# Performance work log

Measured on AMD Instinct MI355X. Metric: run time of the kernel, lower is better.

The kernel has to match this reference:

```python
import jax, jax.numpy as jnp
import numpy as np
import math

D = 2048          # embedding_size
H = 16            # nheads
HD = D // H       # head_dim
S = 2048          # seq_len
B = 2
# SwiGLU hidden per source: int(2*(4*D)/3) rounded up to multiple of 256
FF = 256 * ((int(2 * (4 * D) / 3) + 255) // 256)  # 5632
EPS = 1e-6


def pe_row(seq_len, d_model):
    # PositionalEncoding buffer, but forward uses only pe[:, seq_len-1]
    pos = float(seq_len - 1)
    div = jnp.exp(jnp.arange(0, d_model, 2, dtype=jnp.float32) * (-math.log(10000.0) / d_model))
    row = jnp.zeros((d_model,), jnp.float32)
    row = row.at[0::2].set(jnp.sin(pos * div))
    row = row.at[1::2].set(jnp.cos(pos * div))
    return row  # [D]


def rmsnorm(x, g, eps=EPS):
    xf = x.astype(jnp.float32)
    n = xf * jax.lax.rsqrt(jnp.mean(xf * xf, axis=-1, keepdims=True) + eps)
    return g * n.astype(x.dtype)


def setup_inputs() -> dict:
    key = jax.random.key(0)
    ks = jax.random.split(key, 16)
    sd = 0.02
    x = jax.random.normal(ks[0], (B, S, D), jnp.float32)
    mask = jnp.triu(jnp.ones((S, S), jnp.int32), k=1)[None, None]  # [1,1,S,S], 1 = masked
    return {
        'x': x,
        'mask': mask,
        'qkv_w': jax.random.normal(ks[1], (3 * D, D), jnp.float32) * sd,
        'qkv_b': jnp.zeros((3 * D,), jnp.float32),
        'fc_w': jax.random.normal(ks[2], (D, D), jnp.float32) * sd,
        'fc_b': jnp.zeros((D,), jnp.float32),
        'w1': jax.random.normal(ks[3], (FF, D), jnp.float32) * sd,
        'b1': jnp.zeros((FF,), jnp.float32),
        'w2': jax.random.normal(ks[4], (FF, D), jnp.float32) * sd,
        'b2': jnp.zeros((FF,), jnp.float32),
        'w3': jax.random.normal(ks[5], (D, FF), jnp.float32) * sd,
        'b3': jnp.zeros((D,), jnp.float32),
        'g_attn': jnp.ones((D,), jnp.float32),
        'g_ff': jnp.ones((D,), jnp.float32),
    }


def _block(x, mask, qkv_w, qkv_b, fc_w, fc_b, w1, b1, w2, b2, w3, b3, g_attn, g_ff):
    b, s, _ = x.shape
    # attention sublayer (pre-norm)
    h_in = rmsnorm(x, g_attn)
    qkv = h_in @ qkv_w.T + qkv_b
    xq, xk, xv = jnp.split(qkv, 3, axis=-1)
    pe = pe_row(s, D)  # single row added everywhere (faithful to source)
    xq = xq + pe
    xk = xk + pe
    q = xq.reshape(b, s, H, HD).transpose(0, 2, 1, 3)
    k = xk.reshape(b, s, H, HD).transpose(0, 2, 1, 3)
    v = xv.reshape(b, s, H, HD).transpose(0, 2, 1, 3)
    scores = jnp.einsum('bhqd,bhkd->bhqk', q, k) / math.sqrt(HD)
    scores = jnp.where(mask == 1, jnp.float32(-1e9), scores)
    attn = jax.nn.softmax(scores, axis=-1)
    out = jnp.einsum('bhqk,bhkd->bhqd', attn, v)
    out = out.transpose(0, 2, 1, 3).reshape(b, s, D)
    attn_out = out @ fc_w.T + fc_b
    h = x + attn_out
    # SwiGLU FFN sublayer (pre-norm)
    f_in = rmsnorm(h, g_ff)
    gate = jax.nn.silu(f_in @ w1.T + b1) * (f_in @ w2.T + b2)
    return h + gate @ w3.T + b3


def reference(x, mask, qkv_w, qkv_b, fc_w, fc_b, w1, b1, w2, b2, w3, b3, g_attn, g_ff):
    return _block(x, mask, qkv_w, qkv_b, fc_w, fc_b, w1, b1, w2, b2, w3, b3, g_attn, g_ff)
```

## Files before the change

kernel.cpp:

```cpp
#include <hip/hip_runtime.h>
#include <math.h>


typedef __attribute__((ext_vector_type(8))) short bf16x8;
typedef __attribute__((ext_vector_type(4))) short bf16x4;
typedef __attribute__((ext_vector_type(4))) float f32x4;

#define DEVI __device__ __forceinline__

DEVI unsigned short f2bf(float f) {
  unsigned u = __builtin_bit_cast(unsigned, f);
  u += 0x7FFFu + ((u >> 16) & 1u);
  return (unsigned short)(u >> 16);
}
DEVI float bf2f(unsigned short h) {
  unsigned u = ((unsigned)h) << 16;
  return __builtin_bit_cast(float, u);
}

#define GLL16(g, l) __builtin_amdgcn_global_load_lds( \
    (const __attribute__((address_space(1))) unsigned int*)(const void*)(g), \
    (__attribute__((address_space(3))) unsigned int*)(void*)(l), 16, 0, 0)

__global__ __launch_bounds__(256) void wconv_k(const float* __restrict__ src,
                                               unsigned short* __restrict__ dst,
                                               long n8) {
  long t = (long)blockIdx.x * 256 + threadIdx.x;
  if (t >= n8) return;
  const f32x4* s = (const f32x4*)(src + t * 8);
  f32x4 a = s[0], b = s[1];
  bf16x8 o;
#pragma unroll
  for (int j = 0; j < 4; ++j) {
    o[j]     = (short)f2bf(a[j]);
    o[4 + j] = (short)f2bf(b[j]);
  }
  *(bf16x8*)(dst + t * 8) = o;
}

__global__ void pe_k(float* __restrict__ pe) {
  int c = blockIdx.x * 256 + threadIdx.x;
  if (c >= 2048) return;
  int i2 = c & ~1;
  float div = __expf(-(float)i2 * (9.210340371976184f / 2048.0f));
  float ang = 2047.0f * div;
  pe[c] = (c & 1) ? cosf(ang) : sinf(ang);
}

__global__ __launch_bounds__(256) void rmsnorm_k(const float* __restrict__ x,
                                                 const float* __restrict__ g,
                                                 unsigned short* __restrict__ out) {
  long row = blockIdx.x;
  const float* xr = x + row * 2048;
  int tid = threadIdx.x;
  f32x4 v0 = *(const f32x4*)&xr[tid * 8];
  f32x4 v1 = *(const f32x4*)&xr[tid * 8 + 4];
  float ss = 0.f;
#pragma unroll
  for (int j = 0; j < 4; ++j) ss += v0[j] * v0[j] + v1[j] * v1[j];
#pragma unroll
  for (int m = 1; m < 64; m <<= 1) ss += __shfl_xor(ss, m, 64);
  __shared__ float red[4];
  int lane = tid & 63, wv = tid >> 6;
  if (lane == 0) red[wv] = ss;
  __syncthreads();
  float tot = red[0] + red[1] + red[2] + red[3];
  float rn = rsqrtf(tot * (1.0f / 2048.0f) + 1e-6f);
  const float* gr = g + tid * 8;
  bf16x8 o;
#pragma unroll
  for (int j = 0; j < 4; ++j) {
    o[j]     = (short)f2bf(v0[j] * rn * gr[j]);
    o[4 + j] = (short)f2bf(v1[j] * rn * gr[4 + j]);
  }
  *(bf16x8*)&out[row * 2048 + tid * 8] = o;
}

template <int EPI>
__global__ __launch_bounds__(256) void gemm_bt(const unsigned short* __restrict__ A,
                                               const unsigned short* __restrict__ W,
                                               const float* __restrict__ bias,
                                               const void* __restrict__ residv,
                                               void* __restrict__ outv,
                                               int M, int N, int K) {
  __shared__ __align__(16) unsigned short Ab[3][4096];
  __shared__ __align__(16) unsigned short Bb[3][4096];
  const int tid  = threadIdx.x;
  const int lane = tid & 63;
  const int wv   = tid >> 6;
  const int wr   = wv >> 1;
  const int wc   = wv & 1;
  const int l15  = lane & 15;
  const int lg   = lane >> 4;
  const long tm  = (long)blockIdx.y * 128;
  const long tn  = (long)blockIdx.x * 128;

  const int srw = tid >> 2;
  const int sch = ((tid & 3) ^ ((srw >> 1) & 3)) << 3;
  const unsigned short* gA = A + (tm + srw) * (long)K + sch;
  const unsigned short* gB = W + (tn + srw) * (long)K + sch;
  const long rowstep = 64L * K;

#define STG(slot, kt) do {                                          \
    GLL16(gA + ((long)(kt) << 5), &Ab[slot][wv * 512]);             \
    GLL16(gA + rowstep + ((long)(kt) << 5), &Ab[slot][2048 + wv * 512]); \
    GLL16(gB + ((long)(kt) << 5), &Bb[slot][wv * 512]);             \
    GLL16(gB + rowstep + ((long)(kt) << 5), &Bb[slot][2048 + wv * 512]); \
  } while (0)

  const int KT = K >> 5;
  STG(0, 0); STG(1, 1);
  asm volatile("s_waitcnt vmcnt(4)" ::: "memory");
  __builtin_amdgcn_s_barrier();

  f32x4 acc[4][4] = {};
  const int sw = ((lg ^ ((l15 >> 1) & 3)) << 3);

  for (int t = 0; t < KT; ++t) {
    const unsigned short* lA = &Ab[t % 3][0];
    const unsigned short* lB = &Bb[t % 3][0];
    bf16x8 af[4], bfv[4];
#pragma unroll
    for (int m = 0; m < 4; ++m)
      af[m] = *(const bf16x8*)&lA[(wr * 64 + m * 16 + l15) * 32 + sw];
#pragma unroll
    for (int n = 0; n < 4; ++n)
      bfv[n] = *(const bf16x8*)&lB[(wc * 64 + n * 16 + l15) * 32 + sw];
    if (t + 2 < KT) STG((t + 2) % 3, t + 2);
    __builtin_amdgcn_s_setprio(1);
#pragma unroll
    for (int m = 0; m < 4; ++m)
#pragma unroll
      for (int n = 0; n < 4; ++n)
        acc[m][n] = __builtin_amdgcn_mfma_f32_16x16x32_bf16(af[m], bfv[n], acc[m][n], 0, 0, 0);
    __builtin_amdgcn_s_setprio(0);
    if (t + 2 < KT)      asm volatile("s_waitcnt vmcnt(4)" ::: "memory");
    else if (t + 1 < KT) asm volatile("s_waitcnt vmcnt(0)" ::: "memory");
    __builtin_amdgcn_s_barrier();
  }
#undef STG
  __builtin_amdgcn_sched_barrier(0);

  const long row0 = tm + wr * 64 + ((lane >> 4) << 2);
  const long col0 = tn + wc * 64;
#pragma unroll
  for (int n = 0; n < 4; ++n) {
    const long col = col0 + n * 16 + l15;
    const float bv = bias[col];
#pragma unroll
    for (int m = 0; m < 4; ++m) {
      const long rw = row0 + m * 16;
#pragma unroll
      for (int j = 0; j < 4; ++j) {
        const float v = acc[m][n][j] + bv;
        const long i = (rw + j) * (long)N + col;
        if (EPI == 0) {
          ((unsigned short*)outv)[i] = f2bf(v);
        } else if (EPI == 1) {
          ((float*)outv)[i] = ((const float*)residv)[i] + v;
        } else {
          float f1 = bf2f(((const unsigned short*)residv)[i]);
          float sg = f1 / (1.0f + __expf(-f1));
          ((unsigned short*)outv)[i] = f2bf(sg * v);
        }
      }
    }
  }
}

__global__ __launch_bounds__(256) void krepack_k(const unsigned short* __restrict__ qkv,
                                                 const float* __restrict__ pe,
                                                 unsigned short* __restrict__ kpe) {
  long t = (long)blockIdx.x * 256 + threadIdx.x;
  long idx = t * 8;
  long row = idx >> 11;
  int cd  = (int)(idx & 2047);
  int h = cd >> 7, d = cd & 127;
  long b = row >> 11, s = row & 2047;
  bf16x8 v = *(const bf16x8*)&qkv[row * 6144 + 2048 + cd];
  const float* per = &pe[cd];
#pragma unroll
  for (int j = 0; j < 8; ++j)
    v[j] = (short)f2bf(bf2f((unsigned short)v[j]) + per[j]);
  *(bf16x8*)&kpe[(((b * 16 + h)) * 2048 + s) * 128 + d] = v;
}

__global__ __launch_bounds__(256) void vtrans_k(const unsigned short* __restrict__ qkv,
                                                unsigned short* __restrict__ Vt) {
  const int s0 = blockIdx.x * 64;
  const int d0 = blockIdx.y * 64;
  const int bh = blockIdx.z;
  const long b = bh >> 4;
  const int h = bh & 15;
  __shared__ unsigned short tile[64][76];
  const int t = threadIdx.x;
#pragma unroll
  for (int half = 0; half < 2; ++half) {
    int c = t + half * 256;
    int r = c >> 3;
    int cc = (c & 7) * 8;
    bf16x8 v = *(const bf16x8*)&qkv[(b * 2048 + s0 + r) * 6144 + 4096 + h * 128 + d0 + cc];
#pragma unroll
    for (int j = 0; j < 8; ++j) tile[cc + j][r] = (unsigned short)v[j];
  }
  __syncthreads();
#pragma unroll
  for (int half = 0; half < 2; ++half) {
    int c = t + half * 256;
    int dr = c >> 3;
    int sc = (c & 7) * 8;
    bf16x4 lo = *(const bf16x4*)&tile[dr][sc];
    bf16x4 hi = *(const bf16x4*)&tile[dr][sc + 4];
    bf16x8 v;
#pragma unroll
    for (int j = 0; j < 4; ++j) { v[j] = lo[j]; v[4 + j] = hi[j]; }
    *(bf16x8*)&Vt[((long)bh * 128 + d0 + dr) * 2048 + s0 + sc] = v;
  }
}

__global__ __launch_bounds__(256, 2) void fattn_k(const unsigned short* __restrict__ QKV,
                                                  const float* __restrict__ pe,
                                                  const unsigned short* __restrict__ Kp,
                                                  const unsigned short* __restrict__ Vt,
                                                  unsigned short* __restrict__ O) {
  const int lin = blockIdx.x;
  const int chunk = lin & 7;
  const int idx = lin >> 3;
  const int bh = chunk * 4 + (idx >> 4);
  const int i16 = idx & 15;
  const int qb = (i16 & 1) ? ((i16 - 1) >> 1) : (15 - (i16 >> 1));
  const long b = bh >> 4;
  const int h = bh & 15;
  const int q0 = qb * 128;
  const int tid = threadIdx.x, lane = tid & 63, wv = tid >> 6;
  const int l15 = lane & 15, lg = lane >> 4;
  const int qw = q0 + wv * 32;

  __shared__ __align__(16) unsigned short Kl[2][8192];
  __shared__ __align__(16) unsigned short Vl[2][8192];
  __shared__ __align__(16) unsigned short Plds[4][32][40];

  const float scale = 0.08838834764831845f;
  const unsigned short* Qb = QKV + (b * 2048 + qw) * 6144 + h * 128;
  bf16x8 qf[2][4];
#pragma unroll
  for (int r = 0; r < 2; ++r)
#pragma unroll
    for (int kc = 0; kc < 4; ++kc) {
      bf16x8 v = *(const bf16x8*)&Qb[(r * 16 + l15) * 6144 + kc * 32 + lg * 8];
      const float* per = &pe[h * 128 + kc * 32 + lg * 8];
#pragma unroll
      for (int j = 0; j < 8; ++j)
        v[j] = (short)f2bf((bf2f((unsigned short)v[j]) + per[j]) * scale);
      qf[r][kc] = v;
    }

  const unsigned short* Kg = Kp + (long)bh * 2048 * 128;
  const unsigned short* Vg = Vt + (long)bh * 128 * 2048;

  auto stage = [&](int buf, int key0) {
#pragma unroll
    for (int ld = 0; ld < 4; ++ld) {
      int sr = wv * 16 + ld * 4 + (lane >> 4);
      int sc = ((lane & 15) << 3) ^ ((sr & 7) << 3);
      GLL16(Kg + (long)(key0 + sr) * 128 + sc, &Kl[buf][wv * 2048 + ld * 512]);
      int dr = wv * 32 + ld * 8 + (lane >> 3);
      int dc = ((lane & 7) << 3) ^ ((dr & 7) << 3);
      GLL16(Vg + (long)dr * 2048 + key0 + dc, &Vl[buf][wv * 2048 + ld * 512]);
    }
  };

  f32x4 o[2][8] = {};
  float mr[2][4], sdn[2][4];
#pragma unroll
  for (int r = 0; r < 2; ++r)
#pragma unroll
    for (int j = 0; j < 4; ++j) { mr[r][j] = -1e30f; sdn[r][j] = 0.f; }

  const int nkt = (q0 >> 6) + 2;
  stage(0, 0);
  __syncthreads();
  int cur = 0;
  for (int kt = 0; kt < nkt; ++kt) {
    const int key0 = kt << 6;
    if (kt + 1 < nkt) stage(cur ^ 1, key0 + 64);
    if (key0 <= qw + 31) {
      f32x4 s[2][4] = {};
      __builtin_amdgcn_s_setprio(1);
#pragma unroll
      for (int ks = 0; ks < 4; ++ks) {
        bf16x8 kf[4];
#pragma unroll
        for (int kc = 0; kc < 4; ++kc)
          kf[kc] = *(const bf16x8*)&Kl[cur][(ks * 16 + l15) * 128 +
                                           ((kc * 32 + lg * 8) ^ ((l15 & 7) << 3))];
#pragma unroll
        for (int r = 0; r < 2; ++r)
#pragma unroll
          for (int kc = 0; kc < 4; ++kc)
            s[r][ks] = __builtin_amdgcn_mfma_f32_16x16x32_bf16(qf[r][kc], kf[kc], s[r][ks], 0, 0, 0);
      }
      __builtin_amdgcn_s_setprio(0);
      const bool maskt = (key0 + 63 > qw);
      float pm[2][4];
#pragma unroll
      for (int r = 0; r < 2; ++r)
#pragma unroll
        for (int j = 0; j < 4; ++j) pm[r][j] = -1e30f;
#pragma unroll
      for (int r = 0; r < 2; ++r)
#pragma unroll
        for (int ks = 0; ks < 4; ++ks)
#pragma unroll
          for (int j = 0; j < 4; ++j) {
            float v = s[r][ks][j];
            if (maskt) {
              int qrow = qw + r * 16 + lg * 4 + j;
              int key  = key0 + ks * 16 + l15;
              v = (key <= qrow) ? v : -1e30f;
              s[r][ks][j] = v;
            }
            pm[r][j] = fmaxf(pm[r][j], v);
          }
#pragma unroll
      for (int msk = 1; msk < 16; msk <<= 1)
#pragma unroll
        for (int r = 0; r < 2; ++r)
#pragma unroll
          for (int j = 0; j < 4; ++j) pm[r][j] = fmaxf(pm[r][j], __shfl_xor(pm[r][j], msk, 64));
      bool grow = false;
#pragma unroll
      for (int r = 0; r < 2; ++r)
#pragma unroll
        for (int j = 0; j < 4; ++j) grow = grow || (pm[r][j] > mr[r][j] + 8.0f);
      if (__any(grow)) {
#pragma unroll
        for (int r = 0; r < 2; ++r)
#pragma unroll
          for (int j = 0; j < 4; ++j) {
            float mn = fmaxf(mr[r][j], pm[r][j]);
            float corr = __expf(mr[r][j] - mn);
            mr[r][j] = mn;
            sdn[r][j] *= corr;
#pragma unroll
            for (int nf = 0; nf < 8; ++nf) o[r][nf][j] *= corr;
          }
      }
      float ps[2][4];
#pragma unroll
      for (int r = 0; r < 2; ++r)
#pragma unroll
        for (int j = 0; j < 4; ++j) ps[r][j] = 0.f;
#pragma unroll
      for (int r = 0; r < 2; ++r)
#pragma unroll
        for (int ks = 0; ks < 4; ++ks)
#pragma unroll
          for (int j = 0; j < 4; ++j) {
            float e = __expf(s[r][ks][j] - mr[r][j]);
            s[r][ks][j] = e;
            ps[r][j] += e;
          }
#pragma unroll
      for (int msk = 1; msk < 16; msk <<= 1)
#pragma unroll
        for (int r = 0; r < 2; ++r)
#pragma unroll
          for (int j = 0; j < 4; ++j) ps[r][j] += __shfl_xor(ps[r][j], msk, 64);
#pragma unroll
      for (int r = 0; r < 2; ++r)
#pragma unroll
        for (int j = 0; j < 4; ++j) sdn[r][j] += ps[r][j];
#pragma unroll
      for (int hk = 0; hk < 2; ++hk) {
#pragma unroll
        for (int r = 0; r < 2; ++r)
#pragma unroll
          for (int ks2 = 0; ks2 < 2; ++ks2)
#pragma unroll
            for (int j = 0; j < 4; ++j)
              Plds[wv][r * 16 + lg * 4 + j][ks2 * 16 + l15] = f2bf(s[r][hk * 2 + ks2][j]);
        bf16x8 pf[2];
#pragma unroll
        for (int r = 0; r < 2; ++r) {
          bf16x4 lo = *(const bf16x4*)&Plds[wv][r * 16 + l15][lg * 8];
          bf16x4 hi = *(const bf16x4*)&Plds[wv][r * 16 + l15][lg * 8 + 4];
          bf16x8 p;
#pragma unroll
          for (int j = 0; j < 4; ++j) { p[j] = lo[j]; p[4 + j] = hi[j]; }
          pf[r] = p;
        }
        __builtin_amdgcn_s_setprio(1);
#pragma unroll
        for (int nf = 0; nf < 8; ++nf) {
          bf16x8 vf = *(const bf16x8*)&Vl[cur][(nf * 16 + l15) * 64 +
                                              ((hk * 32 + lg * 8) ^ ((l15 & 7) << 3))];
#pragma unroll
          for (int r = 0; r < 2; ++r)
            o[r][nf] = __builtin_amdgcn_mfma_f32_16x16x32_bf16(pf[r], vf, o[r][nf], 0, 0, 0);
        }
        __builtin_amdgcn_s_setprio(0);
      }
    }
    __syncthreads();
    cur ^= 1;
  }
  unsigned short* Ob = O + (b * 2048 + qw) * 2048 + h * 128;
#pragma unroll
  for (int r = 0; r < 2; ++r)
#pragma unroll
    for (int j = 0; j < 4; ++j) {
      float inv = 1.0f / sdn[r][j];
#pragma unroll
      for (int nf = 0; nf < 8; ++nf)
        Ob[(long)(r * 16 + lg * 4 + j) * 2048 + nf * 16 + l15] = f2bf(o[r][nf][j] * inv);
    }
}

extern "C" void kernel_launch(void* const* d_in, const int* in_sizes, int n_in,
                              void* d_out, int out_size, void* d_ws, size_t ws_size,
                              hipStream_t stream) {
  (void)in_sizes; (void)n_in; (void)out_size; (void)ws_size;
  const float* x    = (const float*)d_in[0];
  const float* qkvw = (const float*)d_in[2];
  const float* qkvb = (const float*)d_in[3];
  const float* fcw  = (const float*)d_in[4];
  const float* fcb  = (const float*)d_in[5];
  const float* w1   = (const float*)d_in[6];
  const float* b1   = (const float*)d_in[7];
  const float* w2   = (const float*)d_in[8];
  const float* b2   = (const float*)d_in[9];
  const float* w3   = (const float*)d_in[10];
  const float* b3   = (const float*)d_in[11];
  const float* ga   = (const float*)d_in[12];
  const float* gf   = (const float*)d_in[13];

  char* ws = (char*)d_ws;
  size_t off = 0;
  auto alloc = [&](size_t bytes) -> char* {
    char* p = ws + off;
    off = (off + bytes + 255) & ~(size_t)255;
    return p;
  };
  unsigned short* wqkv  = (unsigned short*)alloc(6144L * 2048 * 2);
  unsigned short* wfc   = (unsigned short*)alloc(2048L * 2048 * 2);
  unsigned short* w1b   = (unsigned short*)alloc(5632L * 2048 * 2);
  unsigned short* w2b   = (unsigned short*)alloc(5632L * 2048 * 2);
  unsigned short* w3b   = (unsigned short*)alloc(2048L * 5632 * 2);
  float*          pe    = (float*)alloc(2048 * 4);
  unsigned short* hin   = (unsigned short*)alloc(4096L * 2048 * 2);
  unsigned short* qkv   = (unsigned short*)alloc(4096L * 6144 * 2);
  unsigned short* kpe   = (unsigned short*)alloc(4096L * 2048 * 2);
  unsigned short* Vt    = (unsigned short*)alloc(4096L * 2048 * 2);
  unsigned short* attnb = (unsigned short*)alloc(4096L * 2048 * 2);
  float* h = (float*)d_out;

  wconv_k<<<6144, 256, 0, stream>>>(qkvw, wqkv, 6144L * 2048 / 8);
  wconv_k<<<2048, 256, 0, stream>>>(fcw,  wfc,  2048L * 2048 / 8);
  wconv_k<<<5632, 256, 0, stream>>>(w1,   w1b,  5632L * 2048 / 8);
  wconv_k<<<5632, 256, 0, stream>>>(w2,   w2b,  5632L * 2048 / 8);
  wconv_k<<<5632, 256, 0, stream>>>(w3,   w3b,  2048L * 5632 / 8);
  pe_k<<<8, 256, 0, stream>>>(pe);

  rmsnorm_k<<<4096, 256, 0, stream>>>(x, ga, hin);
  gemm_bt<0><<<dim3(48, 32), 256, 0, stream>>>(hin, wqkv, qkvb, nullptr, qkv, 4096, 6144, 2048);
  krepack_k<<<4096, 256, 0, stream>>>(qkv, pe, kpe);
  vtrans_k<<<dim3(32, 2, 32), 256, 0, stream>>>(qkv, Vt);
  fattn_k<<<dim3(512), 256, 0, stream>>>(qkv, pe, kpe, Vt, attnb);
  gemm_bt<1><<<dim3(16, 32), 256, 0, stream>>>(attnb, wfc, fcb, x, h, 4096, 2048, 2048);

  rmsnorm_k<<<4096, 256, 0, stream>>>(h, gf, hin);
  unsigned short* a1 = qkv;
  gemm_bt<0><<<dim3(44, 32), 256, 0, stream>>>(hin, w1b, b1, nullptr, a1, 4096, 5632, 2048);
  gemm_bt<2><<<dim3(44, 32), 256, 0, stream>>>(hin, w2b, b2, a1, a1, 4096, 5632, 2048);
  gemm_bt<1><<<dim3(16, 32), 256, 0, stream>>>(a1, w3b, b3, h, d_out, 4096, 2048, 5632);
}
```

Measured before the change: 760.3 us.

## Fuse SwiGLU gate and up GEMMs into one dual-accumulator kernel

```diff
diff --git a/kernel.cpp b/kernel.cpp
--- a/kernel.cpp
+++ b/kernel.cpp
@@ -156,13 +156,106 @@
         const long i = (rw + j) * (long)N + col;
         if (EPI == 0) {
           ((unsigned short*)outv)[i] = f2bf(v);
-        } else if (EPI == 1) {
+        } else {
           ((float*)outv)[i] = ((const float*)residv)[i] + v;
-        } else {
-          float f1 = bf2f(((const unsigned short*)residv)[i]);
-          float sg = f1 / (1.0f + __expf(-f1));
-          ((unsigned short*)outv)[i] = f2bf(sg * v);
         }
+      }
+    }
+  }
+}
+
+__global__ __launch_bounds__(256, 3) void gemm_ff(const unsigned short* __restrict__ A,
+                                                  const unsigned short* __restrict__ W1,
+                                                  const unsigned short* __restrict__ W2,
+                                                  const float* __restrict__ b1,
+                                                  const float* __restrict__ b2,
+                                                  unsigned short* __restrict__ out,
+                                                  int M, int N, int K) {
+  __shared__ __align__(16) unsigned short Ab[2][4096];
+  __shared__ __align__(16) unsigned short B1b[2][4096];
+  __shared__ __align__(16) unsigned short B2b[2][4096];
+  const int tid  = threadIdx.x;
+  const int lane = tid & 63;
+  const int wv   = tid >> 6;
+  const int wr   = wv >> 1;
+  const int wc   = wv & 1;
+  const int l15  = lane & 15;
+  const int lg   = lane >> 4;
+  const long tm  = (long)blockIdx.y * 128;
+  const long tn  = (long)blockIdx.x * 128;
+
+  const int srw = tid >> 2;
+  const int sch = ((tid & 3) ^ ((srw >> 1) & 3)) << 3;
+  const unsigned short* gA  = A  + (tm + srw) * (long)K + sch;
+  const unsigned short* gB1 = W1 + (tn + srw) * (long)K + sch;
+  const unsigned short* gB2 = W2 + (tn + srw) * (long)K + sch;
+  const long rowstep = 64L * K;
+
+#define STGF(buf, kt) do {                                              \
+    GLL16(gA  + ((long)(kt) << 5), &Ab[buf][wv * 512]);                 \
+    GLL16(gA  + rowstep + ((long)(kt) << 5), &Ab[buf][2048 + wv * 512]); \
+    GLL16(gB1 + ((long)(kt) << 5), &B1b[buf][wv * 512]);                \
+    GLL16(gB1 + rowstep + ((long)(kt) << 5), &B1b[buf][2048 + wv * 512]); \
+    GLL16(gB2 + ((long)(kt) << 5), &B2b[buf][wv * 512]);                \
+    GLL16(gB2 + rowstep + ((long)(kt) << 5), &B2b[buf][2048 + wv * 512]); \
+  } while (0)
+
+  const int KT = K >> 5;
+  STGF(0, 0);
+  f32x4 acc1[4][4] = {}, acc2[4][4] = {};
+  const int sw = ((lg ^ ((l15 >> 1) & 3)) << 3);
+  int cur = 0;
+  for (int t = 0; t < KT; ++t) {
+    __syncthreads();
+    if (t + 1 < KT) STGF(cur ^ 1, t + 1);
+    const unsigned short* lA  = &Ab[cur][0];
+    const unsigned short* lB1 = &B1b[cur][0];
+    const unsigned short* lB2 = &B2b[cur][0];
+    bf16x8 af[4], bfv[4];
+#pragma unroll
+    for (int m = 0; m < 4; ++m)
+      af[m] = *(const bf16x8*)&lA[(wr * 64 + m * 16 + l15) * 32 + sw];
+#pragma unroll
+    for (int n = 0; n < 4; ++n)
+      bfv[n] = *(const bf16x8*)&lB1[(wc * 64 + n * 16 + l15) * 32 + sw];
+    __builtin_amdgcn_s_setprio(1);
+#pragma unroll
+    for (int m = 0; m < 4; ++m)
+#pragma unroll
+      for (int n = 0; n < 4; ++n)
+        acc1[m][n] = __builtin_amdgcn_mfma_f32_16x16x32_bf16(af[m], bfv[n], acc1[m][n], 0, 0, 0);
+    __builtin_amdgcn_s_setprio(0);
+#pragma unroll
+    for (int n = 0; n < 4; ++n)
+      bfv[n] = *(const bf16x8*)&lB2[(wc * 64 + n * 16 + l15) * 32 + sw];
+    __builtin_amdgcn_s_setprio(1);
+#pragma unroll
+    for (int m = 0; m < 4; ++m)
+#pragma unroll
+      for (int n = 0; n < 4; ++n)
+        acc2[m][n] = __builtin_amdgcn_mfma_f32_16x16x32_bf16(af[m], bfv[n], acc2[m][n], 0, 0, 0);
+    __builtin_amdgcn_s_setprio(0);
+    cur ^= 1;
+  }
+#undef STGF
+  __builtin_amdgcn_sched_barrier(0);
+
+  const long row0 = tm + wr * 64 + ((lane >> 4) << 2);
+  const long col0 = tn + wc * 64;
+#pragma unroll
+  for (int n = 0; n < 4; ++n) {
+    const long col = col0 + n * 16 + l15;
+    const float bv1 = b1[col];
+    const float bv2 = b2[col];
+#pragma unroll
+    for (int m = 0; m < 4; ++m) {
+      const long rw = row0 + m * 16;
+#pragma unroll
+      for (int j = 0; j < 4; ++j) {
+        const float v1 = acc1[m][n][j] + bv1;
+        const float v2 = acc2[m][n][j] + bv2;
+        const float sg = v1 / (1.0f + __expf(-v1));
+        out[(rw + j) * (long)N + col] = f2bf(sg * v2);
       }
     }
   }
@@ -471,7 +564,6 @@
 
   rmsnorm_k<<<4096, 256, 0, stream>>>(h, gf, hin);
   unsigned short* a1 = qkv;
-  gemm_bt<0><<<dim3(44, 32), 256, 0, stream>>>(hin, w1b, b1, nullptr, a1, 4096, 5632, 2048);
-  gemm_bt<2><<<dim3(44, 32), 256, 0, stream>>>(hin, w2b, b2, a1, a1, 4096, 5632, 2048);
+  gemm_ff<<<dim3(44, 32), 256, 0, stream>>>(hin, w1b, w2b, b1, b2, a1, 4096, 5632, 2048);
   gemm_bt<1><<<dim3(16, 32), 256, 0, stream>>>(a1, w3b, b3, h, d_out, 4096, 2048, 5632);
 }
```

New measurement: 973.4 us. +28.0%, slower.
